# Optimization experiments

Measured on AMD Instinct MI355X. Metric: run time of the kernel, lower is better.

## Reference

```python
import jax, jax.numpy as jnp
import numpy as np

B, T = 256, 64
VOCAB = 10000
VIS, WORD, RNN = 1024, 512, 512


def setup_inputs() -> dict:
    key = jax.random.key(0)
    ks = jax.random.split(key, 12)
    s = 0.02
    return {
        "vis_feats": jax.random.normal(ks[0], (B, VIS), jnp.float32),
        "seqz": jax.random.randint(ks[1], (B, T), 0, VOCAB, jnp.int32),
        # learned params (x @ W convention, W: [in, out])
        "emb": jax.random.normal(ks[2], (VOCAB + 2, WORD), jnp.float32) * s,
        "W_ih": jax.random.normal(ks[3], (VIS + WORD, 4 * RNN), jnp.float32) * s,
        "W_hh": jax.random.normal(ks[4], (RNN, 4 * RNN), jnp.float32) * s,
        "b_lstm": jnp.zeros((4 * RNN,), jnp.float32),
        "vis2g_W": jax.random.normal(ks[5], (VIS, RNN), jnp.float32) * s,
        "vis2g_b": jnp.zeros((RNN,), jnp.float32),
        "w2g_W": jax.random.normal(ks[6], (WORD, RNN), jnp.float32) * s,
        "h2g_W": jax.random.normal(ks[7], (RNN, RNN), jnp.float32) * s,
        "out_W": jax.random.normal(ks[8], (RNN, VOCAB + 1), jnp.float32) * s,
        "out_b": jnp.zeros((VOCAB + 1,), jnp.float32),
    }


def _decode(vis_feats, seqz, emb, W_ih, W_hh, b_lstm, vis2g_W, vis2g_b,
            w2g_W, h2g_W, out_W, out_b):
    Bn, Tn = seqz.shape
    # input word ids per step: SOS (=vocab+1) at t=0, then seqz[:, t-1]
    sos = jnp.full((1, Bn), VOCAB + 1, seqz.dtype)
    words = jnp.concatenate([sos, seqz[:, :-1].T], axis=0)          # [T, B]
    mask = jnp.concatenate([jnp.ones((1, Bn), jnp.float32),
                            (seqz[:, :-1] != 0).T.astype(jnp.float32)], axis=0)  # [T, B]
    targets = seqz.T                                                 # [T, B]

    def step(carry, xs):
        h, c = carry
        widx, tgt, m = xs
        w = emb[widx]                                   # [B, 512]
        x = jnp.concatenate([vis_feats, w], axis=1)     # [B, 1536]
        gates = x @ W_ih + h @ W_hh + b_lstm            # [B, 2048]
        i_g, f_g, g_g, o_g = jnp.split(gates, 4, axis=1)
        c_new = jax.nn.sigmoid(f_g) * c + jax.nn.sigmoid(i_g) * jnp.tanh(g_g)
        h_new = jax.nn.sigmoid(o_g) * jnp.tanh(c_new)
        # visual-sentinel gate: g = sigmoid(w2g(w) + vis2g(vis) + h2g(h_prev))
        g = jax.nn.sigmoid(w @ w2g_W + vis_feats @ vis2g_W + vis2g_b + h @ h2g_W)
        s_t = g * jnp.tanh(c_new)                       # [B, 512]
        logits = s_t @ out_W + out_b                    # [B, V+1]
        lp = jax.nn.log_softmax(logits, axis=-1) * m[:, None]
        out_t = jnp.take_along_axis(lp, tgt[:, None], axis=1)[:, 0]  # [B]
        return (h_new, c_new), out_t

    init = (jnp.zeros((Bn, RNN), jnp.float32), jnp.zeros((Bn, RNN), jnp.float32))
    _, log_probs = jax.lax.scan(step, init, (words, targets, mask))
    return log_probs  # [T, B]


def reference(vis_feats, seqz, emb, W_ih, W_hh, b_lstm, vis2g_W, vis2g_b,
              w2g_W, h2g_W, out_W, out_b):
    return _decode(vis_feats, seqz, emb, W_ih, W_hh, b_lstm, vis2g_W,
                   vis2g_b, w2g_W, h2g_W, out_W, out_b)
```

## Files before the change

### kernel.cpp

```cpp
#include <hip/hip_runtime.h>
#include <hip/hip_bf16.h>
#include <math.h>

typedef __attribute__((ext_vector_type(8))) short short8;
typedef __attribute__((ext_vector_type(4))) float f32x4;

#define MFMA16(a, b, c) __builtin_amdgcn_mfma_f32_16x16x32_bf16((a), (b), (c), 0, 0, 0)

#define BB 256
#define TT 64
#define VOCAB 10000
#define WORD 512
#define RNN 512
#define NC 2560
#define NV 10001
#define NVP 10016
#define NTILES 626

typedef unsigned long long ull;
union U16 { ull u[2]; short8 s8; };

__device__ __forceinline__ float sigf(float x) { return 1.f / (1.f + __expf(-x)); }
__device__ __forceinline__ float bf2f(short s) {
    union { unsigned int u; float f; } v;
    v.u = ((unsigned int)(unsigned short)s) << 16;
    return v.f;
}
__device__ __forceinline__ short f2bfs(float x) {
    __hip_bfloat16 h = __float2bfloat16(x);
    return *reinterpret_cast<short*>(&h);
}

__device__ __forceinline__ void gload_lds16(const void* g, void* l) {
    __builtin_amdgcn_global_load_lds((const __attribute__((address_space(1))) void*)g,
                                     (__attribute__((address_space(3))) void*)l, 16, 0, 0);
}

__device__ __forceinline__ void stage_tile(const short8* gsrc, void* lbuf, int w, int lane) {
    const char* g = (const char*)gsrc + w * 4096 + lane * 16;
    char* l = (char*)lbuf + w * 4096;
#pragma unroll
    for (int i = 0; i < 4; i++) gload_lds16(g + i * 1024, l + i * 1024);
}


__global__ void transpose_cvt(const float* __restrict__ src, int K, int N, int ld,
                              __hip_bfloat16* __restrict__ dst, int dst_ld, int dstN) {
    __shared__ float tile[32][33];
    int k0 = blockIdx.y * 32, n0 = blockIdx.x * 32;
    int tx = threadIdx.x, ty = threadIdx.y;
#pragma unroll
    for (int i = 0; i < 32; i += 8) {
        int k = k0 + ty + i, n = n0 + tx;
        tile[ty + i][tx] = (k < K && n < N) ? src[(size_t)k * ld + n] : 0.f;
    }
    __syncthreads();
#pragma unroll
    for (int i = 0; i < 32; i += 8) {
        int n = n0 + ty + i, k = k0 + tx;
        if (n < dstN && k < K) dst[(size_t)n * dst_ld + k] = __float2bfloat16(tile[tx][ty + i]);
    }
}

__global__ void swizzle_frag(const short8* __restrict__ src, short8* __restrict__ dst, int ntiles) {
    int t = blockIdx.x * 256 + threadIdx.x;
    if (t >= ntiles * 1024) return;
    int ct = t >> 10, r = t & 1023, kt = r >> 6, l = r & 63;
    int li = l & 15, q = l >> 4;
    dst[t] = src[(size_t)(ct * 16 + li) * 64 + kt * 4 + q];
}

__global__ void zero_state(float* c, __hip_bfloat16* h) {
    int idx = blockIdx.x * 256 + threadIdx.x;
    c[idx] = 0.f;
    h[idx] = __float2bfloat16(0.f);
}

__global__ void cvt_vis(const float* __restrict__ v, __hip_bfloat16* __restrict__ d) {
    int idx = blockIdx.x * 256 + threadIdx.x;
    d[idx] = __float2bfloat16(v[idx]);
}

__global__ __launch_bounds__(256) void gemm_vis(const __hip_bfloat16* __restrict__ A,
                                                const __hip_bfloat16* __restrict__ Bt,
                                                const float* __restrict__ b_lstm,
                                                const float* __restrict__ vis2g_b,
                                                float* __restrict__ C) {
    int wid = blockIdx.x * 4 + (threadIdx.x >> 6);
    int mt = wid / 160, nt = wid % 160;
    int lane = threadIdx.x & 63, li = lane & 15, q = lane >> 4;
    const short8* Ap = (const short8*)A + (mt * 16 + li) * 128 + q;
    const short8* Bp = (const short8*)Bt + (nt * 16 + li) * 128 + q;
    f32x4 acc = {0.f, 0.f, 0.f, 0.f};
#pragma unroll
    for (int kk = 0; kk < 128; kk += 4) acc = MFMA16(Ap[kk], Bp[kk], acc);
    int col = nt * 16 + li;
    float bias = (col < 2048) ? b_lstm[col] : vis2g_b[col - 2048];
#pragma unroll
    for (int r = 0; r < 4; r++) {
        int row = mt * 16 + q * 4 + r;
        C[row * NC + col] = acc[r] + bias;
    }
}

__global__ __launch_bounds__(256) void pre_gemm(const int* __restrict__ seqz,
                                                const float* __restrict__ emb,
                                                const short8* __restrict__ Bsw,
                                                const float* __restrict__ visC,
                                                __hip_bfloat16* __restrict__ preF) {
    __shared__ short8 lds[2][1024];
    int w = threadIdx.x >> 6, lane = threadIdx.x & 63, li = lane & 15, q = lane >> 4;
    int r0 = blockIdx.x * 128 + w * 32;

    short8 a0[16], a1[16];
    {
        int row = r0 + li;
        int t = row >> 8, b = row & 255;
        int wid_ = (t == 0) ? (VOCAB + 1) : seqz[b * TT + (t - 1)];
        const float* er = emb + (size_t)wid_ * WORD + q * 8;
#pragma unroll
        for (int kt = 0; kt < 16; kt++) {
            float4 f0 = ((const float4*)(er + kt * 32))[0];
            float4 f1 = ((const float4*)(er + kt * 32))[1];
            short8 v; v[0]=f2bfs(f0.x); v[1]=f2bfs(f0.y); v[2]=f2bfs(f0.z); v[3]=f2bfs(f0.w);
            v[4]=f2bfs(f1.x); v[5]=f2bfs(f1.y); v[6]=f2bfs(f1.z); v[7]=f2bfs(f1.w);
            a0[kt] = v;
        }
        row = r0 + 16 + li; t = row >> 8; b = row & 255;
        wid_ = (t == 0) ? (VOCAB + 1) : seqz[b * TT + (t - 1)];
        er = emb + (size_t)wid_ * WORD + q * 8;
#pragma unroll
        for (int kt = 0; kt < 16; kt++) {
            float4 f0 = ((const float4*)(er + kt * 32))[0];
            float4 f1 = ((const float4*)(er + kt * 32))[1];
            short8 v; v[0]=f2bfs(f0.x); v[1]=f2bfs(f0.y); v[2]=f2bfs(f0.z); v[3]=f2bfs(f0.w);
            v[4]=f2bfs(f1.x); v[5]=f2bfs(f1.y); v[6]=f2bfs(f1.z); v[7]=f2bfs(f1.w);
            a1[kt] = v;
        }
    }

    int t0 = blockIdx.y * 20, t1 = t0 + 20;
    stage_tile(Bsw + (size_t)t0 * 1024, lds[0], w, lane);
    int ib = 0;
    for (int ct = t0; ct < t1; ++ct, ib ^= 1) {
        __syncthreads();
        if (ct + 1 < t1) stage_tile(Bsw + (size_t)(ct + 1) * 1024, lds[ib ^ 1], w, lane);
        const short8* B = lds[ib];
        f32x4 c0 = {0.f,0.f,0.f,0.f}, c1 = {0.f,0.f,0.f,0.f};
#pragma unroll
        for (int kt = 0; kt < 16; kt++) {
            short8 bv = B[kt * 64 + lane];
            c0 = MFMA16(bv, a0[kt], c0);
            c1 = MFMA16(bv, a1[kt], c1);
        }
        int col0 = ct * 16 + q * 4;
        size_t tb0 = ((size_t)(r0 >> 4) * 160 + ct) * 256 + lane * 4;
        size_t tb1 = tb0 + (size_t)160 * 256;
        float4 v0 = *(const float4*)(visC + ((r0 + li) & 255) * NC + col0);
        float4 v1 = *(const float4*)(visC + ((r0 + 16 + li) & 255) * NC + col0);
        preF[tb0 + 0] = __float2bfloat16(c0[0] + v0.x);
        preF[tb0 + 1] = __float2bfloat16(c0[1] + v0.y);
        preF[tb0 + 2] = __float2bfloat16(c0[2] + v0.z);
        preF[tb0 + 3] = __float2bfloat16(c0[3] + v0.w);
        preF[tb1 + 0] = __float2bfloat16(c1[0] + v1.x);
        preF[tb1 + 1] = __float2bfloat16(c1[1] + v1.y);
        preF[tb1 + 2] = __float2bfloat16(c1[2] + v1.z);
        preF[tb1 + 3] = __float2bfloat16(c1[3] + v1.w);
    }
}

__global__ __launch_bounds__(64, 1) void lstm_persist(const short8* __restrict__ WHsw,
                                                      const __hip_bfloat16* __restrict__ preF,
                                                      __hip_bfloat16* __restrict__ h0,
                                                      __hip_bfloat16* __restrict__ h1,
                                                      __hip_bfloat16* __restrict__ S,
                                                      int* __restrict__ flags) {
    __shared__ short8 ldsB[4096];
    int wid = blockIdx.x;
    int bt = wid & 15, jt = (wid >> 4) & 31;
    int lane = threadIdx.x;
    int li = lane & 15, q = lane >> 4;

#pragma unroll
    for (int g = 0; g < 4; ++g) {
        const char* src = (const char*)(WHsw + (size_t)(g * 32 + jt) * 1024) + lane * 16;
        char* dst = (char*)ldsB + g * 16384;
#pragma unroll
        for (int i = 0; i < 16; ++i) gload_lds16(src + i * 1024, dst + i * 1024);
    }
    short8 b4[16];
    const short8* B4 = WHsw + (size_t)(128 + jt) * 1024 + lane;
#pragma unroll
    for (int kt = 0; kt < 16; ++kt) b4[kt] = B4[kt * 64];
    __syncthreads();

    int* flagp = flags + bt * 64;
    f32x4 cacc = {0.f, 0.f, 0.f, 0.f};

    int hin  = (bt * 16 + li) * 1024 + q * 16;
    int hout = (bt * 16 + li) * 1024 + (jt * 16 + q * 4) * 2;

    const ull* ppw = (const ull*)preF + ((size_t)bt * 160 + jt) * 64 + lane;

    ull ppA[5], ppB[5];
#pragma unroll
    for (int g = 0; g < 5; ++g) ppA[g] = ppw[g * 2048];

#define LSTM_STEP(T, HC, HN, PPC, PPN)                                             \
  {                                                                                \
    if ((T) > 0) {                                                                 \
      int it = 0;                                                                  \
      while (true) {                                                               \
        int v = (T);                                                               \
        if (lane < 32)                                                             \
          v = __hip_atomic_load(flagp + lane, __ATOMIC_RELAXED,                    \
                                __HIP_MEMORY_SCOPE_SYSTEM);                        \
        if (__all(v >= (T))) break;                                                \
        if (++it > 30000) break;               \
        __builtin_amdgcn_s_sleep(1);                                               \
      }                                                                            \
    }                                                                              \
    const ull* hp = (const ull*)((const char*)(HC) + hin);                         \
    ull hf[32];                                                                    \
    _Pragma("unroll") for (int kt = 0; kt < 16; ++kt) {                            \
      hf[2 * kt]     = __hip_atomic_load(hp + kt * 8, __ATOMIC_RELAXED,            \
                                         __HIP_MEMORY_SCOPE_SYSTEM);               \
      hf[2 * kt + 1] = __hip_atomic_load(hp + kt * 8 + 1, __ATOMIC_RELAXED,        \
                                         __HIP_MEMORY_SCOPE_SYSTEM);               \
    }                                                                              \
    if ((T) + 1 < TT) {                                                            \
      const ull* pn = ppw + (size_t)((T) + 1) * 163840;                            \
      _Pragma("unroll") for (int g = 0; g < 5; ++g) (PPN)[g] = pn[g * 2048];       \
    }                                                                              \
    f32x4 g0 = {0.f, 0.f, 0.f, 0.f}, g1 = g0, g2 = g0, g3 = g0, g4 = g0;           \
    _Pragma("unroll") for (int kt = 0; kt < 16; ++kt) {                            \
      U16 hv; hv.u[0] = hf[2 * kt]; hv.u[1] = hf[2 * kt + 1];                      \
      short8 bv = hv.s8;                                                           \
      g0 = MFMA16(ldsB[       kt * 64 + lane], bv, g0);                            \
      g1 = MFMA16(ldsB[1024 + kt * 64 + lane], bv, g1);                            \
      g2 = MFMA16(ldsB[2048 + kt * 64 + lane], bv, g2);                            \
      g3 = MFMA16(ldsB[3072 + kt * 64 + lane], bv, g3);                            \
      g4 = MFMA16(b4[kt], bv, g4);                                                 \
    }                                                                              \
    ull hvout = 0ull, svout = 0ull;                                                \
    _Pragma("unroll") for (int r = 0; r < 4; ++r) {                                \
      float ig = sigf(g0[r] + bf2f((short)((PPC)[0] >> (16 * r))));                \
      float fg = sigf(g1[r] + bf2f((short)((PPC)[1] >> (16 * r))));                \
      float gg = tanhf(g2[r] + bf2f((short)((PPC)[2] >> (16 * r))));               \
      float og = sigf(g3[r] + bf2f((short)((PPC)[3] >> (16 * r))));                \
      float gp = sigf(g4[r] + bf2f((short)((PPC)[4] >> (16 * r))));                \
      float cn = fg * cacc[r] + ig * gg;                                           \
      float tc = tanhf(cn);                                                        \
      cacc[r] = cn;                                                                \
      hvout |= ((ull)(unsigned short)f2bfs(og * tc)) << (16 * r);                  \
      svout |= ((ull)(unsigned short)f2bfs(gp * tc)) << (16 * r);                  \
    }                                                                              \
    __hip_atomic_store((ull*)((char*)(HN) + hout), hvout,                          \
                       __ATOMIC_RELAXED, __HIP_MEMORY_SCOPE_SYSTEM);               \
    *(ull*)((char*)S + (size_t)(T) * 262144 + hout) = svout;                       \
    asm volatile("s_waitcnt vmcnt(0)" ::: "memory");                               \
    if (lane == 0)                                                                 \
      __hip_atomic_store(flagp + jt, (T) + 1, __ATOMIC_RELAXED,                    \
                         __HIP_MEMORY_SCOPE_SYSTEM);                               \
  }

    for (int t = 0; t < TT; t += 2) {
        LSTM_STEP(t,     h0, h1, ppA, ppB);
        LSTM_STEP(t + 1, h1, h0, ppB, ppA);
    }
#undef LSTM_STEP
}


__global__ __launch_bounds__(256) void lse_gemm(const short8* __restrict__ S8,
                                                const short8* __restrict__ Bsw,
                                                const float* __restrict__ ob,
                                                float* __restrict__ sumexp) {
    __shared__ short8 lds[2][1024];
    int w = threadIdx.x >> 6, lane = threadIdx.x & 63, li = lane & 15, q = lane >> 4;
    int r0 = blockIdx.x * 128 + w * 32;
    short8 a0[16], a1[16];
    const short8* Sp0 = S8 + (size_t)(r0 + li) * 64 + q;
    const short8* Sp1 = S8 + (size_t)(r0 + 16 + li) * 64 + q;
#pragma unroll
    for (int kt = 0; kt < 16; kt++) { a0[kt] = Sp0[kt * 4]; a1[kt] = Sp1[kt * 4]; }

    float s0[4] = {0.f,0.f,0.f,0.f}, s1[4] = {0.f,0.f,0.f,0.f};
    int t0 = blockIdx.y * 40;
    int t1 = t0 + 40 < NTILES ? t0 + 40 : NTILES;

    stage_tile(Bsw + (size_t)t0 * 1024, lds[0], w, lane);
    int ib = 0;
    for (int ct = t0; ct < t1; ++ct, ib ^= 1) {
        __syncthreads();
        if (ct + 1 < t1) stage_tile(Bsw + (size_t)(ct + 1) * 1024, lds[ib ^ 1], w, lane);
        const short8* B = lds[ib];
        f32x4 c0 = {0.f,0.f,0.f,0.f}, c1 = {0.f,0.f,0.f,0.f};
#pragma unroll
        for (int kt = 0; kt < 16; kt++) {
            short8 bv = B[kt * 64 + lane];
            c0 = MFMA16(a0[kt], bv, c0);
            c1 = MFMA16(a1[kt], bv, c1);
        }
        int col = ct * 16 + li;
        if (col < NV) {
            float obv = ob[col];
#pragma unroll
            for (int r = 0; r < 4; r++) {
                s0[r] += __expf(c0[r] + obv);
                s1[r] += __expf(c1[r] + obv);
            }
        }
    }
#pragma unroll
    for (int off = 1; off < 16; off <<= 1) {
#pragma unroll
        for (int r = 0; r < 4; r++) { s0[r] += __shfl_xor(s0[r], off); s1[r] += __shfl_xor(s1[r], off); }
    }
    if (li == 0) {
#pragma unroll
        for (int r = 0; r < 4; r++) {
            atomicAdd(&sumexp[r0 + q * 4 + r], s0[r]);
            atomicAdd(&sumexp[r0 + 16 + q * 4 + r], s1[r]);
        }
    }
}

__global__ __launch_bounds__(256) void finalize_k(const __hip_bfloat16* __restrict__ S,
                                                  const __hip_bfloat16* __restrict__ Wt,
                                                  const float* __restrict__ ob,
                                                  const int* __restrict__ seqz,
                                                  const float* __restrict__ sumexp,
                                                  float* __restrict__ out) {
    int w = threadIdx.x >> 6, lane = threadIdx.x & 63;
    int row = blockIdx.x * 4 + w;
    int t = row >> 8, b = row & 255;
    int tgt = seqz[b * TT + t];
    short8 sv = ((const short8*)(S + (size_t)row * 512))[lane];
    short8 wv = ((const short8*)(Wt + (size_t)tgt * 512))[lane];
    float d = 0.f;
#pragma unroll
    for (int i = 0; i < 8; i++) d += bf2f(sv[i]) * bf2f(wv[i]);
#pragma unroll
    for (int off = 1; off < 64; off <<= 1) d += __shfl_xor(d, off);
    if (lane == 0) {
        bool mk = (t == 0) || (seqz[b * TT + t - 1] != 0);
        out[row] = mk ? (d + ob[tgt] - logf(sumexp[row])) : 0.f;
    }
}


extern "C" void kernel_launch(void* const* d_in, const int* in_sizes, int n_in,
                              void* d_out, int out_size, void* d_ws, size_t ws_size,
                              hipStream_t stream) {
    const float* vis     = (const float*)d_in[0];
    const int*   seqz    = (const int*)d_in[1];
    const float* emb     = (const float*)d_in[2];
    const float* W_ih    = (const float*)d_in[3];
    const float* W_hh    = (const float*)d_in[4];
    const float* b_lstm  = (const float*)d_in[5];
    const float* vis2g_W = (const float*)d_in[6];
    const float* vis2g_b = (const float*)d_in[7];
    const float* w2g_W   = (const float*)d_in[8];
    const float* h2g_W   = (const float*)d_in[9];
    const float* out_W   = (const float*)d_in[10];
    const float* out_b   = (const float*)d_in[11];
    float* out = (float*)d_out;

    char* p = (char*)d_ws;
    auto carve = [&](size_t bytes) {
        void* r = (void*)p;
        p += (bytes + 255) & ~(size_t)255;
        return r;
    };
    __hip_bfloat16* WcatW = (__hip_bfloat16*)carve((size_t)NC * 512 * 2);
    __hip_bfloat16* WcatH = (__hip_bfloat16*)carve((size_t)NC * 512 * 2);
    __hip_bfloat16* visWt = (__hip_bfloat16*)carve((size_t)NC * 1024 * 2);
    __hip_bfloat16* outWt = (__hip_bfloat16*)carve((size_t)NVP * 512 * 2);
    short8*         outSw = (short8*)carve((size_t)NTILES * 16384);
    short8*         preBsw= (short8*)carve((size_t)160 * 16384);
    short8*         WHsw  = (short8*)carve((size_t)160 * 16384);
    __hip_bfloat16* visB  = (__hip_bfloat16*)carve((size_t)256 * 1024 * 2);
    float*          visC  = (float*)carve((size_t)256 * NC * 4);
    __hip_bfloat16* preF  = (__hip_bfloat16*)carve((size_t)TT * 256 * NC * 2);
    float*          cbuf  = (float*)carve((size_t)256 * 512 * 4);
    __hip_bfloat16* hb0   = (__hip_bfloat16*)carve((size_t)256 * 512 * 2);
    __hip_bfloat16* hb1   = (__hip_bfloat16*)carve((size_t)256 * 512 * 2);
    __hip_bfloat16* S     = (__hip_bfloat16*)carve((size_t)TT * 256 * 512 * 2);
    float*          sume  = (float*)carve((size_t)TT * 256 * 4);
    int*            bars  = (int*)carve((size_t)16 * 64 * 4);

    dim3 tb(32, 8);
    transpose_cvt<<<dim3(64, 16), tb, 0, stream>>>(W_ih + 1024 * 2048, 512, 2048, 2048, WcatW, 512, 2048);
    transpose_cvt<<<dim3(16, 16), tb, 0, stream>>>(w2g_W, 512, 512, 512, WcatW + 2048 * 512, 512, 512);
    transpose_cvt<<<dim3(64, 16), tb, 0, stream>>>(W_hh, 512, 2048, 2048, WcatH, 512, 2048);
    transpose_cvt<<<dim3(16, 16), tb, 0, stream>>>(h2g_W, 512, 512, 512, WcatH + 2048 * 512, 512, 512);
    transpose_cvt<<<dim3(64, 32), tb, 0, stream>>>(W_ih, 1024, 2048, 2048, visWt, 1024, 2048);
    transpose_cvt<<<dim3(16, 32), tb, 0, stream>>>(vis2g_W, 1024, 512, 512, visWt + 2048 * 1024, 1024, 512);
    transpose_cvt<<<dim3(313, 16), tb, 0, stream>>>(out_W, 512, NV, NV, outWt, 512, NVP);
    swizzle_frag<<<2504, 256, 0, stream>>>((const short8*)outWt, outSw, NTILES);
    swizzle_frag<<<640, 256, 0, stream>>>((const short8*)WcatW, preBsw, 160);
    swizzle_frag<<<640, 256, 0, stream>>>((const short8*)WcatH, WHsw, 160);

    zero_state<<<512, 256, 0, stream>>>(cbuf, hb0);
    cvt_vis<<<1024, 256, 0, stream>>>(vis, visB);
    gemm_vis<<<640, 256, 0, stream>>>(visB, visWt, b_lstm, vis2g_b, visC);
    pre_gemm<<<dim3(128, 8), 256, 0, stream>>>(seqz, emb, preBsw, visC, preF);

    hipMemsetAsync(sume, 0, (size_t)TT * 256 * 4, stream);
    hipMemsetAsync(bars, 0, (size_t)16 * 64 * 4, stream);

    {
        const short8* WHsw_c = (const short8*)WHsw;
        const __hip_bfloat16* preF_c = (const __hip_bfloat16*)preF;
        __hip_bfloat16* h0a = hb0;
        __hip_bfloat16* h1a = hb1;
        __hip_bfloat16* Sa = S;
        int* barsa = bars;
        void* kargs[6] = { &WHsw_c, &preF_c, &h0a, &h1a, &Sa, &barsa };
        hipLaunchCooperativeKernel((void*)lstm_persist, dim3(512), dim3(64), kargs, 0, stream);
    }

    lse_gemm<<<dim3(128, 16), 256, 0, stream>>>((const short8*)S, outSw, out_b, sume);
    finalize_k<<<4096, 256, 0, stream>>>(S, outWt, out_b, seqz, sume, out);
}
```

Measured before the change: 804.1 us.

## Replace flag barrier with sentinel-valued per-step h buffers in persistent LSTM

The persistent LSTM kernel no longer waits on per-block flag counters. Each timestep writes h into its own slice of a (T+1)-slot buffer, pre-filled with 0xFF, and readers spin until none of their loaded h words equal the all-ones sentinel. This removes the separate flag poll, the vmcnt drain and the flag store on each step's critical path. It also swaps in rcp-based sigmoid and a fast exp-based tanh, and remaps the block-to-tile indexing. The cost is about 17 MB of extra memsets and reliance on a bf16 h pair never being 0xFFFF (a NaN bit pattern).

```diff
diff --git a/kernel.cpp b/kernel.cpp
--- a/kernel.cpp
+++ b/kernel.cpp
@@ -20,7 +20,12 @@
 typedef unsigned long long ull;
 union U16 { ull u[2]; short8 s8; };
 
-__device__ __forceinline__ float sigf(float x) { return 1.f / (1.f + __expf(-x)); }
+__device__ __forceinline__ float sigf(float x) {
+    return __builtin_amdgcn_rcpf(1.f + __expf(-x));
+}
+__device__ __forceinline__ float tanhf_fast(float x) {
+    return 1.f - 2.f * __builtin_amdgcn_rcpf(__expf(2.f * x) + 1.f);
+}
 __device__ __forceinline__ float bf2f(short s) {
     union { unsigned int u; float f; } v;
     v.u = ((unsigned int)(unsigned short)s) << 16;
@@ -68,12 +73,6 @@
     int ct = t >> 10, r = t & 1023, kt = r >> 6, l = r & 63;
     int li = l & 15, q = l >> 4;
     dst[t] = src[(size_t)(ct * 16 + li) * 64 + kt * 4 + q];
-}
-
-__global__ void zero_state(float* c, __hip_bfloat16* h) {
-    int idx = blockIdx.x * 256 + threadIdx.x;
-    c[idx] = 0.f;
-    h[idx] = __float2bfloat16(0.f);
 }
 
 __global__ void cvt_vis(const float* __restrict__ v, __hip_bfloat16* __restrict__ d) {
@@ -171,13 +170,11 @@
 
 __global__ __launch_bounds__(64, 1) void lstm_persist(const short8* __restrict__ WHsw,
                                                       const __hip_bfloat16* __restrict__ preF,
-                                                      __hip_bfloat16* __restrict__ h0,
-                                                      __hip_bfloat16* __restrict__ h1,
-                                                      __hip_bfloat16* __restrict__ S,
-                                                      int* __restrict__ flags) {
+                                                      char* __restrict__ hbuf,
+                                                      __hip_bfloat16* __restrict__ S) {
     __shared__ short8 ldsB[4096];
     int wid = blockIdx.x;
-    int bt = wid & 15, jt = (wid >> 4) & 31;
+    int bt = wid >> 5, jt = wid & 31;
     int lane = threadIdx.x;
     int li = lane & 15, q = lane >> 4;
 
@@ -194,7 +191,6 @@
     for (int kt = 0; kt < 16; ++kt) b4[kt] = B4[kt * 64];
     __syncthreads();
 
-    int* flagp = flags + bt * 64;
     f32x4 cacc = {0.f, 0.f, 0.f, 0.f};
 
     int hin  = (bt * 16 + li) * 1024 + q * 16;
@@ -206,27 +202,24 @@
 #pragma unroll
     for (int g = 0; g < 5; ++g) ppA[g] = ppw[g * 2048];
 
-#define LSTM_STEP(T, HC, HN, PPC, PPN)                                             \
+    ull hf[32];
+
+#define LSTM_STEP(T, PPC, PPN)                                                     \
   {                                                                                \
-    if ((T) > 0) {                                                                 \
-      int it = 0;                                                                  \
-      while (true) {                                                               \
-        int v = (T);                                                               \
-        if (lane < 32)                                                             \
-          v = __hip_atomic_load(flagp + lane, __ATOMIC_RELAXED,                    \
-                                __HIP_MEMORY_SCOPE_SYSTEM);                        \
-        if (__all(v >= (T))) break;                                                \
-        if (++it > 30000) break;               \
-        __builtin_amdgcn_s_sleep(1);                                               \
+    const ull* hp = (const ull*)(hbuf + (size_t)(T) * 262144 + hin);               \
+    int it = 0;                                                                    \
+    while (true) {                                                                 \
+      int ok = 1;                                                                  \
+      _Pragma("unroll") for (int kt = 0; kt < 16; ++kt) {                          \
+        hf[2 * kt]     = __hip_atomic_load(hp + kt * 8, __ATOMIC_RELAXED,          \
+                                           __HIP_MEMORY_SCOPE_SYSTEM);             \
+        hf[2 * kt + 1] = __hip_atomic_load(hp + kt * 8 + 1, __ATOMIC_RELAXED,      \
+                                           __HIP_MEMORY_SCOPE_SYSTEM);             \
+        ok &= (hf[2 * kt] != ~0ull) & (hf[2 * kt + 1] != ~0ull);                   \
       }                                                                            \
-    }                                                                              \
-    const ull* hp = (const ull*)((const char*)(HC) + hin);                         \
-    ull hf[32];                                                                    \
-    _Pragma("unroll") for (int kt = 0; kt < 16; ++kt) {                            \
-      hf[2 * kt]     = __hip_atomic_load(hp + kt * 8, __ATOMIC_RELAXED,            \
-                                         __HIP_MEMORY_SCOPE_SYSTEM);               \
-      hf[2 * kt + 1] = __hip_atomic_load(hp + kt * 8 + 1, __ATOMIC_RELAXED,        \
-                                         __HIP_MEMORY_SCOPE_SYSTEM);               \
+      if (__all(ok)) break;                                                        \
+      if (++it > 8000) break;                  \
+      __builtin_amdgcn_s_sleep(1);                                                 \
     }                                                                              \
     if ((T) + 1 < TT) {                                                            \
       const ull* pn = ppw + (size_t)((T) + 1) * 163840;                            \
@@ -246,27 +239,23 @@
     _Pragma("unroll") for (int r = 0; r < 4; ++r) {                                \
       float ig = sigf(g0[r] + bf2f((short)((PPC)[0] >> (16 * r))));                \
       float fg = sigf(g1[r] + bf2f((short)((PPC)[1] >> (16 * r))));                \
-      float gg = tanhf(g2[r] + bf2f((short)((PPC)[2] >> (16 * r))));               \
+      float gg = tanhf_fast(g2[r] + bf2f((short)((PPC)[2] >> (16 * r))));          \
       float og = sigf(g3[r] + bf2f((short)((PPC)[3] >> (16 * r))));                \
       float gp = sigf(g4[r] + bf2f((short)((PPC)[4] >> (16 * r))));                \
       float cn = fg * cacc[r] + ig * gg;                                           \
-      float tc = tanhf(cn);                                                        \
+      float tc = tanhf_fast(cn);                                                   \
       cacc[r] = cn;                                                                \
       hvout |= ((ull)(unsigned short)f2bfs(og * tc)) << (16 * r);                  \
       svout |= ((ull)(unsigned short)f2bfs(gp * tc)) << (16 * r);                  \
     }                                                                              \
-    __hip_atomic_store((ull*)((char*)(HN) + hout), hvout,                          \
+    __hip_atomic_store((ull*)(hbuf + (size_t)((T) + 1) * 262144 + hout), hvout,    \
                        __ATOMIC_RELAXED, __HIP_MEMORY_SCOPE_SYSTEM);               \
     *(ull*)((char*)S + (size_t)(T) * 262144 + hout) = svout;                       \
-    asm volatile("s_waitcnt vmcnt(0)" ::: "memory");                               \
-    if (lane == 0)                                                                 \
-      __hip_atomic_store(flagp + jt, (T) + 1, __ATOMIC_RELAXED,                    \
-                         __HIP_MEMORY_SCOPE_SYSTEM);                               \
   }
 
     for (int t = 0; t < TT; t += 2) {
-        LSTM_STEP(t,     h0, h1, ppA, ppB);
-        LSTM_STEP(t + 1, h1, h0, ppB, ppA);
+        LSTM_STEP(t,     ppA, ppB);
+        LSTM_STEP(t + 1, ppB, ppA);
     }
 #undef LSTM_STEP
 }
@@ -383,12 +372,9 @@
     __hip_bfloat16* visB  = (__hip_bfloat16*)carve((size_t)256 * 1024 * 2);
     float*          visC  = (float*)carve((size_t)256 * NC * 4);
     __hip_bfloat16* preF  = (__hip_bfloat16*)carve((size_t)TT * 256 * NC * 2);
-    float*          cbuf  = (float*)carve((size_t)256 * 512 * 4);
-    __hip_bfloat16* hb0   = (__hip_bfloat16*)carve((size_t)256 * 512 * 2);
-    __hip_bfloat16* hb1   = (__hip_bfloat16*)carve((size_t)256 * 512 * 2);
+    char*           hbuf  = (char*)carve((size_t)(TT + 1) * 262144);
     __hip_bfloat16* S     = (__hip_bfloat16*)carve((size_t)TT * 256 * 512 * 2);
     float*          sume  = (float*)carve((size_t)TT * 256 * 4);
-    int*            bars  = (int*)carve((size_t)16 * 64 * 4);
 
     dim3 tb(32, 8);
     transpose_cvt<<<dim3(64, 16), tb, 0, stream>>>(W_ih + 1024 * 2048, 512, 2048, 2048, WcatW, 512, 2048);
@@ -402,22 +388,20 @@
     swizzle_frag<<<640, 256, 0, stream>>>((const short8*)WcatW, preBsw, 160);
     swizzle_frag<<<640, 256, 0, stream>>>((const short8*)WcatH, WHsw, 160);
 
-    zero_state<<<512, 256, 0, stream>>>(cbuf, hb0);
+    hipMemsetAsync(hbuf, 0, 262144, stream);
+    hipMemsetAsync(hbuf + 262144, 0xFF, (size_t)TT * 262144, stream);
+    hipMemsetAsync(sume, 0, (size_t)TT * 256 * 4, stream);
+
     cvt_vis<<<1024, 256, 0, stream>>>(vis, visB);
     gemm_vis<<<640, 256, 0, stream>>>(visB, visWt, b_lstm, vis2g_b, visC);
     pre_gemm<<<dim3(128, 8), 256, 0, stream>>>(seqz, emb, preBsw, visC, preF);
 
-    hipMemsetAsync(sume, 0, (size_t)TT * 256 * 4, stream);
-    hipMemsetAsync(bars, 0, (size_t)16 * 64 * 4, stream);
-
     {
         const short8* WHsw_c = (const short8*)WHsw;
         const __hip_bfloat16* preF_c = (const __hip_bfloat16*)preF;
-        __hip_bfloat16* h0a = hb0;
-        __hip_bfloat16* h1a = hb1;
+        char* hbufa = hbuf;
         __hip_bfloat16* Sa = S;
-        int* barsa = bars;
-        void* kargs[6] = { &WHsw_c, &preF_c, &h0a, &h1a, &Sa, &barsa };
+        void* kargs[4] = { &WHsw_c, &preF_c, &hbufa, &Sa };
         hipLaunchCooperativeKernel((void*)lstm_persist, dim3(512), dim3(64), kargs, 0, stream);
     }
 
```

Result: slower. 903.5 us (+12.4%).

## Halve persistent LSTM grid by giving each block two batch tiles, use fast tanh

Applied to the files above, without the earlier changes.

The persistent cooperative LSTM kernel now launches 256 single-wave blocks instead of 512. Each block handles two batch tiles (bt and bt+8) for the same hidden tile and reuses the W_hh fragments it has loaded into LDS and registers, interleaving the two half-steps so one tile's flag wait can overlap the other's compute. Sigmoid and tanh switch to rcp/exp approximations, and the zero_state kernel is replaced by memsets. This lowers the number of waves spinning on flags and the per-wave weight staging, but doubles the serial work per wave on the recurrent critical path and slightly reduces activation accuracy.

```diff
diff --git a/kernel.cpp b/kernel.cpp
--- a/kernel.cpp
+++ b/kernel.cpp
@@ -20,7 +20,12 @@
 typedef unsigned long long ull;
 union U16 { ull u[2]; short8 s8; };
 
-__device__ __forceinline__ float sigf(float x) { return 1.f / (1.f + __expf(-x)); }
+__device__ __forceinline__ float sigf(float x) {
+    return __builtin_amdgcn_rcpf(1.f + __expf(-x));
+}
+__device__ __forceinline__ float tanhf_fast(float x) {
+    return 1.f - 2.f * __builtin_amdgcn_rcpf(__expf(2.f * x) + 1.f);
+}
 __device__ __forceinline__ float bf2f(short s) {
     union { unsigned int u; float f; } v;
     v.u = ((unsigned int)(unsigned short)s) << 16;
@@ -68,12 +73,6 @@
     int ct = t >> 10, r = t & 1023, kt = r >> 6, l = r & 63;
     int li = l & 15, q = l >> 4;
     dst[t] = src[(size_t)(ct * 16 + li) * 64 + kt * 4 + q];
-}
-
-__global__ void zero_state(float* c, __hip_bfloat16* h) {
-    int idx = blockIdx.x * 256 + threadIdx.x;
-    c[idx] = 0.f;
-    h[idx] = __float2bfloat16(0.f);
 }
 
 __global__ void cvt_vis(const float* __restrict__ v, __hip_bfloat16* __restrict__ d) {
@@ -177,7 +176,8 @@
                                                       int* __restrict__ flags) {
     __shared__ short8 ldsB[4096];
     int wid = blockIdx.x;
-    int bt = wid & 15, jt = (wid >> 4) & 31;
+    int btA = wid >> 5, jt = wid & 31;
+    int btB = btA + 8;
     int lane = threadIdx.x;
     int li = lane & 15, q = lane >> 4;
 
@@ -194,34 +194,41 @@
     for (int kt = 0; kt < 16; ++kt) b4[kt] = B4[kt * 64];
     __syncthreads();
 
-    int* flagp = flags + bt * 64;
-    f32x4 cacc = {0.f, 0.f, 0.f, 0.f};
-
-    int hin  = (bt * 16 + li) * 1024 + q * 16;
-    int hout = (bt * 16 + li) * 1024 + (jt * 16 + q * 4) * 2;
-
-    const ull* ppw = (const ull*)preF + ((size_t)bt * 160 + jt) * 64 + lane;
-
-    ull ppA[5], ppB[5];
-#pragma unroll
-    for (int g = 0; g < 5; ++g) ppA[g] = ppw[g * 2048];
-
-#define LSTM_STEP(T, HC, HN, PPC, PPN)                                             \
+    int* flagA = flags + btA * 64;
+    int* flagB = flags + btB * 64;
+    f32x4 caccA = {0.f, 0.f, 0.f, 0.f};
+    f32x4 caccB = {0.f, 0.f, 0.f, 0.f};
+
+    int hinA  = (btA * 16 + li) * 1024 + q * 16;
+    int hinB  = (btB * 16 + li) * 1024 + q * 16;
+    int houtA = (btA * 16 + li) * 1024 + (jt * 16 + q * 4) * 2;
+    int houtB = (btB * 16 + li) * 1024 + (jt * 16 + q * 4) * 2;
+
+    const ull* ppwA = (const ull*)preF + ((size_t)btA * 160 + jt) * 64 + lane;
+    const ull* ppwB = (const ull*)preF + ((size_t)btB * 160 + jt) * 64 + lane;
+
+    ull ppAc[5], ppAn[5], ppBc[5], ppBn[5];
+#pragma unroll
+    for (int g = 0; g < 5; ++g) { ppAc[g] = ppwA[g * 2048]; ppBc[g] = ppwB[g * 2048]; }
+
+    ull hf[32];
+
+#define LSTM_HALF(T, FLAGP, HIN, HOUT, CACC, PPC, PPN, PPW, HC, HN)                \
   {                                                                                \
     if ((T) > 0) {                                                                 \
       int it = 0;                                                                  \
       while (true) {                                                               \
         int v = (T);                                                               \
         if (lane < 32)                                                             \
-          v = __hip_atomic_load(flagp + lane, __ATOMIC_RELAXED,                    \
+          v = __hip_atomic_load((FLAGP) + lane, __ATOMIC_RELAXED,                  \
                                 __HIP_MEMORY_SCOPE_SYSTEM);                        \
         if (__all(v >= (T))) break;                                                \
         if (++it > 30000) break;               \
         __builtin_amdgcn_s_sleep(1);                                               \
       }                                                                            \
     }                                                                              \
-    const ull* hp = (const ull*)((const char*)(HC) + hin);                         \
-    ull hf[32];                                                                    \
+    asm volatile("" ::: "memory");   \
+    const ull* hp = (const ull*)((const char*)(HC) + (HIN));                       \
     _Pragma("unroll") for (int kt = 0; kt < 16; ++kt) {                            \
       hf[2 * kt]     = __hip_atomic_load(hp + kt * 8, __ATOMIC_RELAXED,            \
                                          __HIP_MEMORY_SCOPE_SYSTEM);               \
@@ -229,7 +236,7 @@
                                          __HIP_MEMORY_SCOPE_SYSTEM);               \
     }                                                                              \
     if ((T) + 1 < TT) {                                                            \
-      const ull* pn = ppw + (size_t)((T) + 1) * 163840;                            \
+      const ull* pn = (PPW) + (size_t)((T) + 1) * 163840;                          \
       _Pragma("unroll") for (int g = 0; g < 5; ++g) (PPN)[g] = pn[g * 2048];       \
     }                                                                              \
     f32x4 g0 = {0.f, 0.f, 0.f, 0.f}, g1 = g0, g2 = g0, g3 = g0, g4 = g0;           \
@@ -246,29 +253,31 @@
     _Pragma("unroll") for (int r = 0; r < 4; ++r) {                                \
       float ig = sigf(g0[r] + bf2f((short)((PPC)[0] >> (16 * r))));                \
       float fg = sigf(g1[r] + bf2f((short)((PPC)[1] >> (16 * r))));                \
-      float gg = tanhf(g2[r] + bf2f((short)((PPC)[2] >> (16 * r))));               \
+      float gg = tanhf_fast(g2[r] + bf2f((short)((PPC)[2] >> (16 * r))));          \
       float og = sigf(g3[r] + bf2f((short)((PPC)[3] >> (16 * r))));                \
       float gp = sigf(g4[r] + bf2f((short)((PPC)[4] >> (16 * r))));                \
-      float cn = fg * cacc[r] + ig * gg;                                           \
-      float tc = tanhf(cn);                                                        \
-      cacc[r] = cn;                                                                \
+      float cn = fg * (CACC)[r] + ig * gg;                                         \
+      float tc = tanhf_fast(cn);                                                   \
+      (CACC)[r] = cn;                                                              \
       hvout |= ((ull)(unsigned short)f2bfs(og * tc)) << (16 * r);                  \
       svout |= ((ull)(unsigned short)f2bfs(gp * tc)) << (16 * r);                  \
     }                                                                              \
-    __hip_atomic_store((ull*)((char*)(HN) + hout), hvout,                          \
+    __hip_atomic_store((ull*)((char*)(HN) + (HOUT)), hvout,                        \
                        __ATOMIC_RELAXED, __HIP_MEMORY_SCOPE_SYSTEM);               \
-    *(ull*)((char*)S + (size_t)(T) * 262144 + hout) = svout;                       \
+    *(ull*)((char*)S + (size_t)(T) * 262144 + (HOUT)) = svout;                     \
     asm volatile("s_waitcnt vmcnt(0)" ::: "memory");                               \
     if (lane == 0)                                                                 \
-      __hip_atomic_store(flagp + jt, (T) + 1, __ATOMIC_RELAXED,                    \
+      __hip_atomic_store((FLAGP) + jt, (T) + 1, __ATOMIC_RELAXED,                  \
                          __HIP_MEMORY_SCOPE_SYSTEM);                               \
   }
 
     for (int t = 0; t < TT; t += 2) {
-        LSTM_STEP(t,     h0, h1, ppA, ppB);
-        LSTM_STEP(t + 1, h1, h0, ppB, ppA);
-    }
-#undef LSTM_STEP
+        LSTM_HALF(t,     flagA, hinA, houtA, caccA, ppAc, ppAn, ppwA, h0, h1);
+        LSTM_HALF(t,     flagB, hinB, houtB, caccB, ppBc, ppBn, ppwB, h0, h1);
+        LSTM_HALF(t + 1, flagA, hinA, houtA, caccA, ppAn, ppAc, ppwA, h1, h0);
+        LSTM_HALF(t + 1, flagB, hinB, houtB, caccB, ppBn, ppBc, ppwB, h1, h0);
+    }
+#undef LSTM_HALF
 }
 
 
@@ -383,7 +392,6 @@
     __hip_bfloat16* visB  = (__hip_bfloat16*)carve((size_t)256 * 1024 * 2);
     float*          visC  = (float*)carve((size_t)256 * NC * 4);
     __hip_bfloat16* preF  = (__hip_bfloat16*)carve((size_t)TT * 256 * NC * 2);
-    float*          cbuf  = (float*)carve((size_t)256 * 512 * 4);
     __hip_bfloat16* hb0   = (__hip_bfloat16*)carve((size_t)256 * 512 * 2);
     __hip_bfloat16* hb1   = (__hip_bfloat16*)carve((size_t)256 * 512 * 2);
     __hip_bfloat16* S     = (__hip_bfloat16*)carve((size_t)TT * 256 * 512 * 2);
@@ -402,13 +410,13 @@
     swizzle_frag<<<640, 256, 0, stream>>>((const short8*)WcatW, preBsw, 160);
     swizzle_frag<<<640, 256, 0, stream>>>((const short8*)WcatH, WHsw, 160);
 
-    zero_state<<<512, 256, 0, stream>>>(cbuf, hb0);
+    hipMemsetAsync(hb0, 0, (size_t)256 * 512 * 2, stream);
+    hipMemsetAsync(bars, 0, (size_t)16 * 64 * 4, stream);
+    hipMemsetAsync(sume, 0, (size_t)TT * 256 * 4, stream);
+
     cvt_vis<<<1024, 256, 0, stream>>>(vis, visB);
     gemm_vis<<<640, 256, 0, stream>>>(visB, visWt, b_lstm, vis2g_b, visC);
     pre_gemm<<<dim3(128, 8), 256, 0, stream>>>(seqz, emb, preBsw, visC, preF);
-
-    hipMemsetAsync(sume, 0, (size_t)TT * 256 * 4, stream);
-    hipMemsetAsync(bars, 0, (size_t)16 * 64 * 4, stream);
 
     {
         const short8* WHsw_c = (const short8*)WHsw;
@@ -418,7 +426,7 @@
         __hip_bfloat16* Sa = S;
         int* barsa = bars;
         void* kargs[6] = { &WHsw_c, &preF_c, &h0a, &h1a, &Sa, &barsa };
-        hipLaunchCooperativeKernel((void*)lstm_persist, dim3(512), dim3(64), kargs, 0, stream);
+        hipLaunchCooperativeKernel((void*)lstm_persist, dim3(256), dim3(64), kargs, 0, stream);
     }
 
     lse_gemm<<<dim3(128, 16), 256, 0, stream>>>((const short8*)S, outSw, out_b, sume);
```

Result: no change. 807.5 us (+0.4%).
